# Performance work log

Measured on AMD Instinct MI355X. Metric: run time of the kernel, lower is better.

## Reference

```python
import jax, jax.numpy as jnp
import numpy as np

EPS = 1e-6
H, KV, D = 16, 4, 128  # num_heads, num_kv_heads, head_dim
ROPE_BASE = 1000000.0


def rmsnorm(x, w):
    # weight_offset = 1.0: scale is (w + 1)
    var = jnp.mean(x * x, axis=-1, keepdims=True)
    return x * jax.lax.rsqrt(var + EPS) * (w + 1.0)


def rope_tables(S, dtype):
    inv_freq = 1.0 / (ROPE_BASE ** (np.arange(0, D, 2, dtype=np.float32) / D))
    freqs = np.outer(np.arange(S, dtype=np.float32), inv_freq)  # [S, D/2]
    emb = np.concatenate([freqs, freqs], axis=-1)  # [S, D]
    return jnp.asarray(np.cos(emb), dtype), jnp.asarray(np.sin(emb), dtype)


def rotate_half(x):
    x1, x2 = jnp.split(x, 2, axis=-1)
    return jnp.concatenate([-x2, x1], axis=-1)


def setup_inputs() -> dict:
    key = jax.random.key(0)
    ks = jax.random.split(key, 5)
    B, S, HID = 2, 2048, 2048
    return {
        "x": jax.random.normal(ks[0], (B, S, HID), jnp.float32),
        "Wq": jax.random.normal(ks[1], (HID, 2 * H * D), jnp.float32) * 0.02,
        "Wk": jax.random.normal(ks[2], (HID, KV * D), jnp.float32) * 0.02,
        "Wv": jax.random.normal(ks[3], (HID, KV * D), jnp.float32) * 0.02,
        "Wo": jax.random.normal(ks[4], (H * D, HID), jnp.float32) * 0.02,
        "qn_w": jnp.zeros((D,), jnp.float32),
        "kn_w": jnp.zeros((D,), jnp.float32),
    }


def reference(x, Wq, Wk, Wv, Wo, qn_w, kn_w):
    B, S, _ = x.shape
    G = H // KV  # GQA group size
    # projections
    q_raw = (x @ Wq).reshape(B, S, H, 2 * D)
    q, gate = q_raw[..., :D], q_raw[..., D:]
    k = (x @ Wk).reshape(B, S, KV, D)
    v = (x @ Wv).reshape(B, S, KV, D)
    # QK RMSNorm (per head_dim)
    q = rmsnorm(q, qn_w)
    k = rmsnorm(k, kn_w)
    # RoPE (rotate-half form)
    cos, sin = rope_tables(S, x.dtype)  # [S, D]
    c = cos[None, :, None, :]
    s = sin[None, :, None, :]
    q = q * c + rotate_half(q) * s
    k = k * c + rotate_half(k) * s
    # grouped attention: avoid materializing repeated K/V
    # q: [B,S,H,D] -> [B,KV,G,S,D]; head h = kv*G + g matches repeat_interleave
    qg = q.transpose(0, 2, 1, 3).reshape(B, KV, G, S, D)
    kt = k.transpose(0, 2, 1, 3)  # [B,KV,S,D]
    vt = v.transpose(0, 2, 1, 3)  # [B,KV,S,D]
    scale = 1.0 / np.sqrt(D)
    scores = jnp.einsum("bkgsd,bktd->bkgst", qg, kt) * scale  # [B,KV,G,S,S]
    causal = jnp.tril(jnp.ones((S, S), bool))
    scores = jnp.where(causal, scores, jnp.finfo(scores.dtype).min)
    probs = jax.nn.softmax(scores, axis=-1)
    out = jnp.einsum("bkgst,bktd->bkgsd", probs, vt)  # [B,KV,G,S,D]
    out = out.reshape(B, H, S, D)
    # sigmoid gating from q projection
    gate = gate.transpose(0, 2, 1, 3)  # [B,H,S,D]
    out = out * jax.nn.sigmoid(gate)
    out = out.transpose(0, 2, 1, 3).reshape(B, S, H * D)
    return out @ Wo
```

## Files before the change

kernel.cpp:

```cpp
#include <hip/hip_runtime.h>
#include <hip/hip_bf16.h>

typedef unsigned short u16;
typedef __bf16 bf16x8 __attribute__((ext_vector_type(8)));
typedef float f32x4 __attribute__((ext_vector_type(4)));
typedef float f32x16 __attribute__((ext_vector_type(16)));

#define B_   2
#define S_   2048
#define HID_ 2048
#define H_   16
#define KV_  4
#define D_   128
#define TS_  5120

template <int V> struct ic { static constexpr int value = V; };

__device__ __forceinline__ u16 f2b(float f) {
  unsigned u = __float_as_uint(f);
  return (u16)((u + 0x7fffu + ((u >> 16) & 1u)) >> 16);
}
__device__ __forceinline__ float b2f(u16 h) {
  return __uint_as_float(((unsigned)h) << 16);
}
__device__ __forceinline__ unsigned pk2(float a, float b) {
  __hip_bfloat162 h = __float22bfloat162_rn(make_float2(a, b));
  unsigned u;
  __builtin_memcpy(&u, &h, 4);
  return u;
}
__device__ __forceinline__ void cstore(float* p, float v) { *p = v; }
__device__ __forceinline__ void cstore(u16* p, float v)   { *p = f2b(v); }

__device__ __forceinline__ void gl_lds16(const u16* g, u16* l) {
  __builtin_amdgcn_global_load_lds(
      (const __attribute__((address_space(1))) unsigned int*)g,
      (__attribute__((address_space(3))) unsigned int*)l, 16, 0, 0);
}


__global__ __launch_bounds__(256)
void prep0_kernel(const float* __restrict__ Wq, const float* __restrict__ Wk,
                  const float* __restrict__ Wv, const float* __restrict__ Wo,
                  const float* __restrict__ x, u16* __restrict__ Wqt,
                  u16* __restrict__ Wkvt, u16* __restrict__ Wot,
                  u16* __restrict__ xb) {
  __shared__ u16 t[32][33];
  const int tid = threadIdx.x;
  int idx = blockIdx.x;
  if (idx >= 14336) {
    idx -= 14336;
    const int gi = idx * 256 + tid;
    const int r = gi >> 8;
    const int k = (gi & 255) << 3;
    const float4 v0 = *(const float4*)(x + (size_t)r * 2048 + k);
    const float4 v1 = *(const float4*)(x + (size_t)r * 2048 + k + 4);
    uint4 w;
    w.x = pk2(v0.x, v0.y); w.y = pk2(v0.z, v0.w);
    w.z = pk2(v1.x, v1.y); w.w = pk2(v1.z, v1.w);
    const size_t off =
        ((((size_t)(r >> 4) * 64 + (k >> 5)) * 64) + ((k >> 3) & 3) * 16 +
         (r & 15)) * 8;
    *(uint4*)(xb + off) = w;
    return;
  }
  const float* in; u16* out; int Cc, bx, by;
  if (idx < 8192)       { in = Wq; out = Wqt; Cc = 4096; bx = idx & 127; by = idx >> 7; }
  else if (idx < 9216)  { idx -= 8192; in = Wk; out = Wkvt; Cc = 512; bx = idx & 15; by = idx >> 4; }
  else if (idx < 10240) { idx -= 9216; in = Wv; out = Wkvt + (size_t)512 * 2048; Cc = 512; bx = idx & 15; by = idx >> 4; }
  else                  { idx -= 10240; in = Wo; out = Wot; Cc = 2048; bx = idx & 63; by = idx >> 6; }
  const int R = 2048;
  const int tx = tid & 31, ty = tid >> 5;
  const int c0 = bx * 32, r0 = by * 32;
#pragma unroll
  for (int i = 0; i < 4; i++)
    t[ty + i * 8][tx] = f2b(in[(size_t)(r0 + ty + i * 8) * Cc + c0 + tx]);
  __syncthreads();
  if (tid < 128) {
    const int tl = tid >> 6, l = tid & 63, li = l & 15, quad = l >> 4;
    u16 vals[8];
#pragma unroll
    for (int e = 0; e < 8; e++) vals[e] = t[quad * 8 + e][tl * 16 + li];
    const size_t off =
        ((((size_t)(c0 >> 4) + tl) * (R >> 5) + (r0 >> 5)) * 64 + quad * 16 +
         li) * 8;
    *(uint4*)(out + off) = *(const uint4*)vals;
  }
}

__device__ __forceinline__ void rmsrope_body(
    int relblk, int tid, const u16* __restrict__ in,
    const float* __restrict__ w, u16* __restrict__ out, int n_heads,
    int head_stride, float scale) {
  const int warp = (relblk << 2) + (tid >> 6);
  const int lane = tid & 63;
  const int h = warp % n_heads;
  const int tok = warp / n_heads;
  const int s = tok & (S_ - 1);
  const int b = tok >> 11;
  const u16* src = in + (size_t)tok * TS_ + (size_t)h * head_stride;
  float x1 = b2f(src[lane]);
  float x2 = b2f(src[lane + 64]);
  float ss = x1 * x1 + x2 * x2;
#pragma unroll
  for (int off = 1; off < 64; off <<= 1) ss += __shfl_xor(ss, off);
  const float inv = rsqrtf(ss * (1.0f / 128.0f) + 1e-6f) * scale;
  x1 *= inv * (w[lane] + 1.0f);
  x2 *= inv * (w[lane + 64] + 1.0f);
  const float invf = exp2f((float)lane * (-19.931568569324174f / 64.0f));
  const float ang = (float)s * invf;
  float sn, c;
  sincosf(ang, &sn, &c);
  const int wq = lane >> 4, hi = (lane >> 3) & 1, e = lane & 7;
  const size_t tb = (((size_t)b * n_heads + h) * 64 + (s >> 5)) * 4096;
  const size_t o1 = tb + (size_t)(wq * 64 + hi * 32 + (s & 31)) * 8 + e;
  out[o1]        = f2b(x1 * c - x2 * sn);
  out[o1 + 2048] = f2b(x2 * c + x1 * sn);
}

__global__ __launch_bounds__(256)
void prep1_kernel(const u16* __restrict__ qkraw, const float* __restrict__ qn,
                  const float* __restrict__ kn, u16* __restrict__ Qr,
                  u16* __restrict__ Kr, u16* __restrict__ Vtb) {
  const int tid = threadIdx.x;
  int blk = blockIdx.x;
  if (blk < 16384) {
    rmsrope_body(blk, tid, qkraw, qn, Qr, 16, 256, 0.08838834764831845f);
    return;
  }
  blk -= 16384;
  if (blk < 4096) {
    rmsrope_body(blk, tid, qkraw + 4096, kn, Kr, 4, 128, 1.0f);
    return;
  }
  blk -= 4096;
  __shared__ u16 t[32][33];
  const int tx = tid & 31, ty = tid >> 5;
  const int jt = blk & 63, dt = (blk >> 6) & 3, z = blk >> 8;
  const int s0 = jt * 32, d0 = dt * 32;
  const int b = z >> 2, kv = z & 3;
  const u16* in = qkraw + 4096 + 512;
#pragma unroll
  for (int i = 0; i < 4; i++)
    t[ty + i * 8][tx] =
        in[(size_t)(b * S_ + s0 + ty + i * 8) * TS_ + kv * D_ + d0 + tx];
  __syncthreads();
  if (tid < 128) {
    const int kk = tid >> 6, hi2 = (tid >> 5) & 1, d31 = tid & 31;
    u16 vals[8];
#pragma unroll
    for (int e = 0; e < 8; e++) vals[e] = t[kk * 16 + hi2 * 8 + e][d31];
    const size_t off =
        ((((size_t)(b * KV_ + kv) * 64 + jt) * 8 + dt * 2 + kk) * 64 +
         hi2 * 32 + d31) * 8;
    *(uint4*)(Vtb + off) = *(const uint4*)vals;
  }
}

template <typename CT>
__global__ __launch_bounds__(256)
void gemm_nt(const u16* __restrict__ A, const u16* __restrict__ Bt,
             CT* __restrict__ C, int Md, int Nd, int Kd) {
  __shared__ u16 As[2][8 * 512];
  __shared__ u16 Bs[2][8 * 512];
  const int tid = threadIdx.x;
  const int lane = tid & 63;
  const int wave = tid >> 6;
  const int wm = wave >> 1, wn = wave & 1;
  const int li = lane & 15, quad = lane >> 4;

  const int id = blockIdx.x;
  const int grp = id & 7;
  const int r = id >> 3;
  const int px = Nd >> 10;
  const int m0 = (r / px) * 128;
  const int n0 = (grp * px + (r % px)) * 128;

  f32x4 acc[4][4];
#pragma unroll
  for (int i = 0; i < 4; i++)
#pragma unroll
    for (int j = 0; j < 4; j++) acc[i][j] = (f32x4){0.f, 0.f, 0.f, 0.f};

  const size_t ts = (size_t)(Kd >> 5) * 512;
  const u16* Ab = A + ((size_t)(m0 >> 4) + wave * 2) * ts + lane * 8;
  const u16* Bb = Bt + ((size_t)(n0 >> 4) + wave * 2) * ts + lane * 8;

  auto stage = [&](int buf, int k0) {
    const size_t ko = (size_t)k0 * 16;
    gl_lds16(Ab + ko, &As[buf][(wave * 2) * 512]);
    gl_lds16(Ab + ts + ko, &As[buf][(wave * 2 + 1) * 512]);
    gl_lds16(Bb + ko, &Bs[buf][(wave * 2) * 512]);
    gl_lds16(Bb + ts + ko, &Bs[buf][(wave * 2 + 1) * 512]);
  };

  stage(0, 0);
  int cur = 0;
  for (int k0 = 0; k0 < Kd; k0 += 32) {
    __syncthreads();
    if (k0 + 32 < Kd) stage(cur ^ 1, k0 + 32);
    bf16x8 af[4], bfr[4];
#pragma unroll
    for (int mt = 0; mt < 4; mt++)
      af[mt] = *(const bf16x8*)&As[cur][(wm * 4 + mt) * 512 + lane * 8];
#pragma unroll
    for (int nt = 0; nt < 4; nt++)
      bfr[nt] = *(const bf16x8*)&Bs[cur][(wn * 4 + nt) * 512 + lane * 8];
#pragma unroll
    for (int mt = 0; mt < 4; mt++)
#pragma unroll
      for (int nt = 0; nt < 4; nt++)
        acc[mt][nt] = __builtin_amdgcn_mfma_f32_16x16x32_bf16(
            af[mt], bfr[nt], acc[mt][nt], 0, 0, 0);
    cur ^= 1;
  }
#pragma unroll
  for (int mt = 0; mt < 4; mt++) {
    const int row = m0 + wm * 64 + mt * 16 + quad * 4;
#pragma unroll
    for (int nt = 0; nt < 4; nt++) {
      const int col = n0 + wn * 64 + nt * 16 + li;
#pragma unroll
      for (int r2 = 0; r2 < 4; r2++)
        cstore(&C[(size_t)(row + r2) * Nd + col], acc[mt][nt][r2]);
    }
  }
}

__global__ __launch_bounds__(128, 2)
void attn_kernel(const u16* __restrict__ Q, const u16* __restrict__ Kr,
                 const u16* __restrict__ Vt, const u16* __restrict__ qraw,
                 u16* __restrict__ Ag) {
  __shared__ __align__(16) float Wscr[2][2176];
  __shared__ float Mdump[2][32], Ldump[2][32];

  const int tid = threadIdx.x;
  const int lane = tid & 63;
  const int wv = tid >> 6;
  const int l31 = lane & 31, hi = lane >> 5;

  const int id = blockIdx.x;
  const int grp = id & 7;
  const int b = grp >> 2, kv = grp & 3;
  const int rest = id >> 3;
  const int hh = rest & 3;
  const int t = 63 - (rest >> 2);
  const int h = (kv << 2) | hh;
  const int bh = (b << 4) | h;
  const int rs = t * 32;

  const u16* Qb = Q + ((size_t)bh * 64 + t) * 4096;
  const u16* Kb = Kr + (size_t)(b * KV_ + kv) * 64 * 4096;
  const u16* Vb = Vt + (size_t)(b * KV_ + kv) * 64 * 4096;

  bf16x8 qf[8];
#pragma unroll
  for (int w = 0; w < 8; w++)
    qf[w] = *(const bf16x8*)(Qb + w * 512 + lane * 8);

  float m_s = -1e30f, l_s = 0.f;
  f32x16 oacc[4];
#pragma unroll
  for (int dt = 0; dt < 4; dt++)
#pragma unroll
    for (int i = 0; i < 16; i++) oacc[dt][i] = 0.f;

  const int h0 = (t + 2) >> 1;
  const int klo = wv ? h0 : 0;
  const int khi = wv ? (t + 1) : h0;

  bf16x8 kf[8];
  auto loadK = [&](int jt) {
    const u16* kp = Kb + (size_t)jt * 4096 + lane * 8;
#pragma unroll
    for (int w = 0; w < 8; w++) kf[w] = *(const bf16x8*)(kp + w * 512);
  };

  auto step = [&](int jt) {
    const u16* vp = Vb + (size_t)jt * 4096 + lane * 8;
    bf16x8 vf[8];
#pragma unroll
    for (int f = 0; f < 8; f++)
      vf[f] = *(const bf16x8*)(vp + f * 512);

    f32x16 s0, s1;
#pragma unroll
    for (int i = 0; i < 16; i++) { s0[i] = 0.f; s1[i] = 0.f; }
    __builtin_amdgcn_s_setprio(1);
#pragma unroll
    for (int dc = 0; dc < 4; dc++) {
      s0 = __builtin_amdgcn_mfma_f32_32x32x16_bf16(kf[2 * dc], qf[2 * dc], s0,
                                                   0, 0, 0);
      s1 = __builtin_amdgcn_mfma_f32_32x32x16_bf16(kf[2 * dc + 1],
                                                   qf[2 * dc + 1], s1, 0, 0, 0);
    }
    __builtin_amdgcn_s_setprio(0);
    if (jt + 1 < khi) loadK(jt + 1);
    f32x16 s = s0 + s1;

    if (jt == t) {
#pragma unroll
      for (int r = 0; r < 16; r++) {
        const int kl = (r & 3) + 8 * (r >> 2) + 4 * hi;
        if (kl > l31) s[r] = -1e30f;
      }
    }
    float mx4[4];
#pragma unroll
    for (int g = 0; g < 4; g++)
      mx4[g] = fmaxf(fmaxf(s[4 * g], s[4 * g + 1]),
                     fmaxf(s[4 * g + 2], s[4 * g + 3]));
    float mx = fmaxf(fmaxf(mx4[0], mx4[1]), fmaxf(mx4[2], mx4[3]));
    mx = fmaxf(mx, __shfl_xor(mx, 32));
    const bool defer = __all(mx - m_s <= 8.f);
    const float mn = defer ? m_s : fmaxf(m_s, mx);
    if (!defer) {
      const float alpha = __expf(m_s - mn);
      m_s = mn;
      l_s *= alpha;
#pragma unroll
      for (int dt = 0; dt < 4; dt++)
#pragma unroll
        for (int i = 0; i < 16; i++) oacc[dt][i] *= alpha;
    }
    float rs4[4];
#pragma unroll
    for (int g = 0; g < 4; g++) {
      float e0 = __expf(s[4 * g + 0] - mn);
      float e1 = __expf(s[4 * g + 1] - mn);
      float e2 = __expf(s[4 * g + 2] - mn);
      float e3 = __expf(s[4 * g + 3] - mn);
      s[4 * g + 0] = e0; s[4 * g + 1] = e1;
      s[4 * g + 2] = e2; s[4 * g + 3] = e3;
      rs4[g] = (e0 + e1) + (e2 + e3);
    }
    float rsum = (rs4[0] + rs4[1]) + (rs4[2] + rs4[3]);
    rsum += __shfl_xor(rsum, 32);
    l_s += rsum;
    unsigned a0 = pk2(s[0], s[1]),  b0 = pk2(s[2], s[3]);
    unsigned c0 = pk2(s[4], s[5]),  d0 = pk2(s[6], s[7]);
    unsigned e0 = pk2(s[8], s[9]),  f0 = pk2(s[10], s[11]);
    unsigned g0 = pk2(s[12], s[13]), h0w = pk2(s[14], s[15]);
    unsigned r1 = __shfl_xor(hi ? a0 : c0, 32);
    unsigned r2 = __shfl_xor(hi ? b0 : d0, 32);
    unsigned r3 = __shfl_xor(hi ? e0 : g0, 32);
    unsigned r4 = __shfl_xor(hi ? f0 : h0w, 32);
    union U16B { unsigned u[4]; bf16x8 v; };
    U16B p0, p1;
    p0.u[0] = hi ? r1 : a0;  p0.u[1] = hi ? r2 : b0;
    p0.u[2] = hi ? c0 : r1;  p0.u[3] = hi ? d0 : r2;
    p1.u[0] = hi ? r3 : e0;  p1.u[1] = hi ? r4 : f0;
    p1.u[2] = hi ? g0 : r3;  p1.u[3] = hi ? h0w : r4;
    __builtin_amdgcn_s_setprio(1);
#pragma unroll
    for (int dt = 0; dt < 4; dt++) {
      oacc[dt] = __builtin_amdgcn_mfma_f32_32x32x16_bf16(vf[dt * 2], p0.v,
                                                         oacc[dt], 0, 0, 0);
      oacc[dt] = __builtin_amdgcn_mfma_f32_32x32x16_bf16(vf[dt * 2 + 1], p1.v,
                                                         oacc[dt], 0, 0, 0);
    }
    __builtin_amdgcn_s_setprio(0);
  };

  if (klo < khi) {
    loadK(klo);
    for (int jt = klo; jt < khi; jt++) step(jt);
  }

  float* myscr = &Wscr[wv][0];
  auto dumpO = [&](auto wvc) {
    constexpr int WV = decltype(wvc)::value;
#pragma unroll
    for (int i = 0; i < 2; i++) {
#pragma unroll
      for (int g = 0; g < 4; g++) {
        f32x4 w;
        w[0] = oacc[(1 - WV) * 2 + i][4 * g + 0];
        w[1] = oacc[(1 - WV) * 2 + i][4 * g + 1];
        w[2] = oacc[(1 - WV) * 2 + i][4 * g + 2];
        w[3] = oacc[(1 - WV) * 2 + i][4 * g + 3];
        *(f32x4*)&myscr[l31 * 68 + i * 32 + 8 * g + 4 * hi] = w;
      }
    }
    if (hi == 0) {
      Mdump[WV][l31] = m_s;
      Ldump[WV][l31] = l_s;
    }
  };
  if (wv == 0) dumpO(ic<0>{}); else dumpO(ic<1>{});
  __syncthreads();
  auto finO = [&](auto wvc) {
    constexpr int WV = decltype(wvc)::value;
    const float* oscr = &Wscr[1 - WV][0];
    const float mo = Mdump[1 - WV][l31];
    const float lo2 = Ldump[1 - WV][l31];
    const float mm = fmaxf(m_s, mo);
    const float as = __expf(m_s - mm), ao = __expf(mo - mm);
    const float linv = 1.f / (l_s * as + lo2 * ao);
    const size_t tok = (size_t)b * S_ + rs + l31;
    const u16* gp = qraw + tok * TS_ + h * 256 + 128;
#pragma unroll
    for (int i = 0; i < 2; i++) {
#pragma unroll
      for (int g = 0; g < 4; g++) {
        const int dbase = (WV * 2 + i) * 32 + 8 * g + 4 * hi;
        const int dg = h * 128 + dbase;
        f32x4 oo = *(const f32x4*)&oscr[l31 * 68 + i * 32 + 8 * g + 4 * hi];
        uint2 gv = *(const uint2*)(gp + dbase);
        float g0 = b2f((u16)(gv.x & 0xffff)), g1 = b2f((u16)(gv.x >> 16));
        float g2 = b2f((u16)(gv.y & 0xffff)), g3 = b2f((u16)(gv.y >> 16));
        float o0 = (oacc[WV * 2 + i][4 * g + 0] * as + oo[0] * ao) * linv /
                   (1.f + __expf(-g0));
        float o1 = (oacc[WV * 2 + i][4 * g + 1] * as + oo[1] * ao) * linv /
                   (1.f + __expf(-g1));
        float o2 = (oacc[WV * 2 + i][4 * g + 2] * as + oo[2] * ao) * linv /
                   (1.f + __expf(-g2));
        float o3 = (oacc[WV * 2 + i][4 * g + 3] * as + oo[3] * ao) * linv /
                   (1.f + __expf(-g3));
        const size_t off =
            (((tok >> 4) * 64 + (dg >> 5)) * 64 + ((dg >> 3) & 3) * 16 +
             (tok & 15)) * 8 + 4 * hi;
        *(uint2*)(Ag + off) = make_uint2(pk2(o0, o1), pk2(o2, o3));
      }
    }
  };
  if (wv == 0) finO(ic<0>{}); else finO(ic<1>{});
}

extern "C" void kernel_launch(void* const* d_in, const int* in_sizes, int n_in,
                              void* d_out, int out_size, void* d_ws,
                              size_t ws_size, hipStream_t stream) {
  const float* x  = (const float*)d_in[0];
  const float* Wq = (const float*)d_in[1];
  const float* Wk = (const float*)d_in[2];
  const float* Wv = (const float*)d_in[3];
  const float* Wo = (const float*)d_in[4];
  const float* qn = (const float*)d_in[5];
  const float* kn = (const float*)d_in[6];
  float* out = (float*)d_out;
  char* ws = (char*)d_ws;

  u16* xb    = (u16*)(ws + 0);
  u16* Wqt   = (u16*)(ws + 16777216);
  u16* Wkvt  = (u16*)(ws + 33554432);
  u16* Wot   = (u16*)(ws + 37748736);
  u16* qkraw = (u16*)(ws + 46137344);
  u16* Vtb   = (u16*)(ws + 88080384);
  u16* Kr    = (u16*)(ws + 92274688);
  u16* Ag    = (u16*)(ws + 96468992);
  u16* Qr = xb;

  prep0_kernel<<<18432, 256, 0, stream>>>(Wq, Wk, Wv, Wo, x, Wqt, Wkvt, Wot, xb);

  gemm_nt<u16><<<1280, 256, 0, stream>>>(xb, Wqt, qkraw, 4096, TS_, 2048);

  prep1_kernel<<<22528, 256, 0, stream>>>(qkraw, qn, kn, Qr, Kr, Vtb);

  attn_kernel<<<2048, 128, 0, stream>>>(Qr, Kr, Vtb, qkraw, Ag);
  gemm_nt<float><<<512, 256, 0, stream>>>(Ag, Wot, out, 4096, 2048, 2048);
}
```

Baseline: 363.4 us.

## Split attention KV range across four waves with LDS cross-wave merge

```diff
diff --git a/kernel.cpp b/kernel.cpp
--- a/kernel.cpp
+++ b/kernel.cpp
@@ -227,12 +227,12 @@
   }
 }
 
-__global__ __launch_bounds__(128, 2)
+__global__ __launch_bounds__(256, 3)
 void attn_kernel(const u16* __restrict__ Q, const u16* __restrict__ Kr,
                  const u16* __restrict__ Vt, const u16* __restrict__ qraw,
                  u16* __restrict__ Ag) {
-  __shared__ __align__(16) float Wscr[2][2176];
-  __shared__ float Mdump[2][32], Ldump[2][32];
+  __shared__ float Oex[12][32 * 33];
+  __shared__ float Mdump[4][32], Ldump[4][32];
 
   const int tid = threadIdx.x;
   const int lane = tid & 63;
@@ -265,9 +265,8 @@
 #pragma unroll
     for (int i = 0; i < 16; i++) oacc[dt][i] = 0.f;
 
-  const int h0 = (t + 2) >> 1;
-  const int klo = wv ? h0 : 0;
-  const int khi = wv ? (t + 1) : h0;
+  const int klo = ((t + 1) * wv) >> 2;
+  const int khi = ((t + 1) * (wv + 1)) >> 2;
 
   bf16x8 kf[8];
   auto loadK = [&](int jt) {
@@ -367,64 +366,79 @@
     for (int jt = klo; jt < khi; jt++) step(jt);
   }
 
-  float* myscr = &Wscr[wv][0];
+  if (hi == 0) {
+    Mdump[wv][l31] = m_s;
+    Ldump[wv][l31] = l_s;
+  }
   auto dumpO = [&](auto wvc) {
     constexpr int WV = decltype(wvc)::value;
 #pragma unroll
-    for (int i = 0; i < 2; i++) {
-#pragma unroll
-      for (int g = 0; g < 4; g++) {
-        f32x4 w;
-        w[0] = oacc[(1 - WV) * 2 + i][4 * g + 0];
-        w[1] = oacc[(1 - WV) * 2 + i][4 * g + 1];
-        w[2] = oacc[(1 - WV) * 2 + i][4 * g + 2];
-        w[3] = oacc[(1 - WV) * 2 + i][4 * g + 3];
-        *(f32x4*)&myscr[l31 * 68 + i * 32 + 8 * g + 4 * hi] = w;
-      }
-    }
-    if (hi == 0) {
-      Mdump[WV][l31] = m_s;
-      Ldump[WV][l31] = l_s;
+    for (int dt = 0; dt < 4; dt++) {
+      if (dt == WV) continue;
+      const int slot = dt * 3 + (WV > dt ? WV - 1 : WV);
+      float* dst = &Oex[slot][l31 * 33];
+#pragma unroll
+      for (int g = 0; g < 4; g++)
+#pragma unroll
+        for (int j = 0; j < 4; j++)
+          dst[8 * g + 4 * hi + j] = oacc[dt][4 * g + j];
     }
   };
-  if (wv == 0) dumpO(ic<0>{}); else dumpO(ic<1>{});
+  if (wv == 0) dumpO(ic<0>{});
+  else if (wv == 1) dumpO(ic<1>{});
+  else if (wv == 2) dumpO(ic<2>{});
+  else dumpO(ic<3>{});
   __syncthreads();
   auto finO = [&](auto wvc) {
     constexpr int WV = decltype(wvc)::value;
-    const float* oscr = &Wscr[1 - WV][0];
-    const float mo = Mdump[1 - WV][l31];
-    const float lo2 = Ldump[1 - WV][l31];
-    const float mm = fmaxf(m_s, mo);
-    const float as = __expf(m_s - mm), ao = __expf(mo - mm);
-    const float linv = 1.f / (l_s * as + lo2 * ao);
+    const float m01 = fmaxf(Mdump[0][l31], Mdump[1][l31]);
+    const float m23 = fmaxf(Mdump[2][l31], Mdump[3][l31]);
+    const float mstar = fmaxf(m01, m23);
+    float al[4];
+    float L = 0.f;
+#pragma unroll
+    for (int u = 0; u < 4; u++) {
+      al[u] = __expf(Mdump[u][l31] - mstar);
+      L += Ldump[u][l31] * al[u];
+    }
+    const float linv = 1.f / L;
+    float ov[16];
+#pragma unroll
+    for (int i2 = 0; i2 < 16; i2++) ov[i2] = oacc[WV][i2] * al[WV];
+#pragma unroll
+    for (int u = 0; u < 4; u++) {
+      if (u == WV) continue;
+      const int slot = WV * 3 + (u > WV ? u - 1 : u);
+      const float* src = &Oex[slot][l31 * 33];
+#pragma unroll
+      for (int g = 0; g < 4; g++)
+#pragma unroll
+        for (int j = 0; j < 4; j++)
+          ov[4 * g + j] += al[u] * src[8 * g + 4 * hi + j];
+    }
     const size_t tok = (size_t)b * S_ + rs + l31;
     const u16* gp = qraw + tok * TS_ + h * 256 + 128;
 #pragma unroll
-    for (int i = 0; i < 2; i++) {
-#pragma unroll
-      for (int g = 0; g < 4; g++) {
-        const int dbase = (WV * 2 + i) * 32 + 8 * g + 4 * hi;
-        const int dg = h * 128 + dbase;
-        f32x4 oo = *(const f32x4*)&oscr[l31 * 68 + i * 32 + 8 * g + 4 * hi];
-        uint2 gv = *(const uint2*)(gp + dbase);
-        float g0 = b2f((u16)(gv.x & 0xffff)), g1 = b2f((u16)(gv.x >> 16));
-        float g2 = b2f((u16)(gv.y & 0xffff)), g3 = b2f((u16)(gv.y >> 16));
-        float o0 = (oacc[WV * 2 + i][4 * g + 0] * as + oo[0] * ao) * linv /
-                   (1.f + __expf(-g0));
-        float o1 = (oacc[WV * 2 + i][4 * g + 1] * as + oo[1] * ao) * linv /
-                   (1.f + __expf(-g1));
-        float o2 = (oacc[WV * 2 + i][4 * g + 2] * as + oo[2] * ao) * linv /
-                   (1.f + __expf(-g2));
-        float o3 = (oacc[WV * 2 + i][4 * g + 3] * as + oo[3] * ao) * linv /
-                   (1.f + __expf(-g3));
-        const size_t off =
-            (((tok >> 4) * 64 + (dg >> 5)) * 64 + ((dg >> 3) & 3) * 16 +
-             (tok & 15)) * 8 + 4 * hi;
-        *(uint2*)(Ag + off) = make_uint2(pk2(o0, o1), pk2(o2, o3));
-      }
+    for (int g = 0; g < 4; g++) {
+      const int dbase = WV * 32 + 8 * g + 4 * hi;
+      const int dg = h * 128 + dbase;
+      uint2 gv = *(const uint2*)(gp + dbase);
+      float g0 = b2f((u16)(gv.x & 0xffff)), g1 = b2f((u16)(gv.x >> 16));
+      float g2 = b2f((u16)(gv.y & 0xffff)), g3 = b2f((u16)(gv.y >> 16));
+      float o0 = ov[4 * g + 0] * linv / (1.f + __expf(-g0));
+      float o1 = ov[4 * g + 1] * linv / (1.f + __expf(-g1));
+      float o2 = ov[4 * g + 2] * linv / (1.f + __expf(-g2));
+      float o3 = ov[4 * g + 3] * linv / (1.f + __expf(-g3));
+      const size_t off =
+          (((tok >> 4) * 64 + (dg >> 5)) * 64 + ((dg >> 3) & 3) * 16 +
+           (tok & 15)) * 8 + 4 * hi;
+      *(uint2*)(Ag + off) = make_uint2(pk2(o0, o1), pk2(o2, o3));
     }
   };
-  if (wv == 0) finO(ic<0>{}); else finO(ic<1>{});
+  if (wv == 0) finO(ic<0>{});
+  else if (wv == 1) finO(ic<1>{});
+  else if (wv == 2) finO(ic<2>{});
+  else finO(ic<3>{});
 }
 
 extern "C" void kernel_launch(void* const* d_in, const int* in_sizes, int n_in,
@@ -456,6 +470,6 @@
 
   prep1_kernel<<<22528, 256, 0, stream>>>(qkraw, qn, kn, Qr, Kr, Vtb);
 
-  attn_kernel<<<2048, 128, 0, stream>>>(Qr, Kr, Vtb, qkraw, Ag);
+  attn_kernel<<<2048, 256, 0, stream>>>(Qr, Kr, Vtb, qkraw, Ag);
   gemm_nt<float><<<512, 256, 0, stream>>>(Ag, Wot, out, 4096, 2048, 2048);
 }
```

Measured after the change: 493.1 us. +35.7%, slower.
